# Kernel optimization log

Hardware: AMD Instinct MI355X
Metric: run time of the kernel (lower is better)

Reference implementation:

```python
import jax, jax.numpy as jnp
import numpy as np

D_K = 64
N_STEPS = 4
NEG = -1e9  # stand-in for -inf; keeps vjp NaN-free, numerically identical softmax


def setup_inputs() -> dict:
    key = jax.random.key(0)
    ks = jax.random.split(key, 12)
    B, N, D = 4, 2048, 1024
    s = 0.02
    return {
        "hidden": jax.random.normal(ks[0], (B, N, D), jnp.float32),
        "W1": jax.random.normal(ks[1], (64, D), jnp.float32) * s,
        "b1": jnp.zeros((64,), jnp.float32),
        "W2": jax.random.normal(ks[2], (28, 64), jnp.float32) * s,
        "b2": jnp.zeros((28,), jnp.float32),
        "Wq": jax.random.normal(ks[3], (D_K, 28), jnp.float32) * s,
        "Wk": jax.random.normal(ks[4], (D_K, 28), jnp.float32) * s,
        "Wc": jax.random.normal(ks[5], (1, 28), jnp.float32) * s,
        "bc": jnp.zeros((1,), jnp.float32),
        "Wv": jax.random.normal(ks[6], (D_K, D), jnp.float32) * s,
        "Wo": jax.random.normal(ks[7], (D, D_K), jnp.float32) * s,  # torch inits this to zeros; randomized for a non-trivial baseline
        "step_size": jnp.asarray(0.5, jnp.float32),
        "charge_decay": jnp.asarray(0.3, jnp.float32),
        "layer_idx": 0,
    }


def reference(hidden, W1, b1, W2, b2, Wq, Wk, Wc, bc, Wv, Wo, step_size, charge_decay, layer_idx):
    B, N, D = hidden.shape
    # features come from detached hidden in the torch code
    h_sg = jax.lax.stop_gradient(hidden)
    f = jax.nn.gelu(h_sg @ W1.T + b1, approximate=False)  # [B,N,64]
    features = jax.nn.sigmoid(f @ W2.T + b2)              # [B,N,28]
    Q = features @ Wq.T                                   # [B,N,64]
    K = features @ Wk.T                                   # [B,N,64]
    compat = jnp.einsum('bnd,bmd->bnm', Q, K) / jnp.float32(np.sqrt(D_K))
    charge = jax.nn.sigmoid(features @ Wc.T + bc)[..., 0]  # [B,N]
    causal = jnp.tril(jnp.ones((N, N), dtype=bool))
    logits = jnp.where(causal, compat, NEG)
    for _ in range(N_STEPS):
        attn = jax.nn.softmax(logits, axis=-1)            # [B,N,N]
        received = attn.sum(axis=-2)                      # [B,N]
        charge = charge * (1.0 - charge_decay * jax.nn.sigmoid(received - 1.0))
        energy = -compat * charge[:, :, None] * charge[:, None, :]
        logits = jnp.where(causal, logits - step_size * energy, NEG)
    attn = jax.nn.softmax(logits, axis=-1)
    V = hidden @ Wv.T                                     # [B,N,64]
    out = jnp.einsum('bnm,bmd->bnd', attn, V) @ Wo.T      # [B,N,D]
    return out * 0.1
```

## Files before the change

### kernel.cpp

```cpp
#include <hip/hip_runtime.h>
#include <hip/hip_bf16.h>

typedef unsigned short ushort_t;
typedef short bf16x8 __attribute__((ext_vector_type(8)));
typedef ushort_t u16x8 __attribute__((ext_vector_type(8)));
typedef float f32x4 __attribute__((ext_vector_type(4)));

#define DEV static __device__ __forceinline__

DEV float bf2f(ushort_t u) { unsigned v = ((unsigned)u) << 16; float f; __builtin_memcpy(&f, &v, 4); return f; }
DEV short f2bf(float x) { __hip_bfloat16 h = __float2bfloat16(x); short s; __builtin_memcpy(&s, &h, 2); return s; }
DEV float sigm(float x) { return 1.0f / (1.0f + __expf(-x)); }

DEV bf16x8 cvt8(float4 a0, float4 a1) {
    bf16x8 t;
    t[0] = f2bf(a0.x); t[1] = f2bf(a0.y); t[2] = f2bf(a0.z); t[3] = f2bf(a0.w);
    t[4] = f2bf(a1.x); t[5] = f2bf(a1.y); t[6] = f2bf(a1.z); t[7] = f2bf(a1.w);
    return t;
}
DEV bf16x8 ld8f(const float* __restrict__ p) {
    return cvt8(*reinterpret_cast<const float4*>(p), *reinterpret_cast<const float4*>(p + 4));
}

__global__ void k_cvt(const float* __restrict__ src, ushort_t* __restrict__ dst, int n8) {
    int i = blockIdx.x * 256 + threadIdx.x;
    if (i >= n8) return;
    const float4* p = reinterpret_cast<const float4*>(src) + (long)i * 2;
    *reinterpret_cast<bf16x8*>(dst + (long)i * 8) = cvt8(p[0], p[1]);
}

__global__ __launch_bounds__(256) void k_fv(const ushort_t* __restrict__ Hb,
        const ushort_t* __restrict__ Wcat,
        float* __restrict__ Ff, ushort_t* __restrict__ VbT) {
    int m0 = blockIdx.x * 16;
    int wave = threadIdx.x >> 6, lane = threadIdx.x & 63;
    int l16 = lane & 15, quad = lane >> 4;
    int cb = (wave & 1) * 32;
    int brow_off = (wave < 2) ? 0 : 64;
    f32x4 acc[2] = {};
    const ushort_t* arow = Hb + (long)(m0 + l16) * 1024;
    const ushort_t* brow0 = Wcat + (long)(brow_off + cb + l16) * 1024;
    const ushort_t* brow1 = Wcat + (long)(brow_off + cb + 16 + l16) * 1024;
    for (int kc = 0; kc < 1024; kc += 128) {
        bf16x8 a4[4], b04[4], b14[4];
#pragma unroll
        for (int u = 0; u < 4; u++) {
            int ko = kc + u * 32 + quad * 8;
            a4[u] = *reinterpret_cast<const bf16x8*>(arow + ko);
            b04[u] = *reinterpret_cast<const bf16x8*>(brow0 + ko);
            b14[u] = *reinterpret_cast<const bf16x8*>(brow1 + ko);
        }
#pragma unroll
        for (int u = 0; u < 4; u++) {
            acc[0] = __builtin_amdgcn_mfma_f32_16x16x32_bf16(a4[u], b04[u], acc[0], 0, 0, 0);
            acc[1] = __builtin_amdgcn_mfma_f32_16x16x32_bf16(a4[u], b14[u], acc[1], 0, 0, 0);
        }
    }
    bool isV = (wave >= 2);
#pragma unroll
    for (int c = 0; c < 2; c++)
#pragma unroll
        for (int rr = 0; rr < 4; rr++) {
            int row = m0 + quad * 4 + rr;
            int col = cb + c * 16 + l16;
            float v = acc[c][rr];
            if (!isV) Ff[row * 64 + col] = v;
            else VbT[(long)col * 8192 + row] = (ushort_t)f2bf(v);
        }
}

__global__ __launch_bounds__(256) void k_feat(const float* __restrict__ Ff,
        const float* __restrict__ b1, const float* __restrict__ W2, const float* __restrict__ b2,
        const float* __restrict__ Wq, const float* __restrict__ Wk,
        const float* __restrict__ Wc, const float* __restrict__ bc,
        ushort_t* __restrict__ Qb, ushort_t* __restrict__ Kb,
        float* __restrict__ charge0, float* __restrict__ received) {
    __shared__ float w2L[28 * 65], wqL[64 * 29], wkL[64 * 29], wcL[28], b2L[28];
    __shared__ float fL[4][64], featL[4][28];
    int tid = threadIdx.x;
    for (int i = tid; i < 28 * 64; i += 256) w2L[(i >> 6) * 65 + (i & 63)] = W2[i];
    for (int i = tid; i < 64 * 28; i += 256) {
        int r = i / 28, c = i - r * 28;
        wqL[r * 29 + c] = Wq[i];
        wkL[r * 29 + c] = Wk[i];
    }
    if (tid < 28) { wcL[tid] = Wc[tid]; b2L[tid] = b2[tid]; }
    __syncthreads();
    int w = tid >> 6, lane = tid & 63;
    float b1v = b1[lane];
    float bcv = bc[0];
    for (int it = 0; it < 8; it++) {
        int row = blockIdx.x * 32 + it * 4 + w;
        float x = Ff[row * 64 + lane] + b1v;
        fL[w][lane] = 0.5f * x * (1.0f + erff(x * 0.70710678118654752f));
        __syncthreads();
        if (lane < 28) {
            float s = b2L[lane];
#pragma unroll
            for (int j = 0; j < 64; j++) s += fL[w][j] * w2L[lane * 65 + j];
            featL[w][lane] = sigm(s);
        }
        __syncthreads();
        float q = 0.f, k = 0.f;
#pragma unroll
        for (int i = 0; i < 28; i++) {
            float fv = featL[w][i];
            q += fv * wqL[lane * 29 + i];
            k += fv * wkL[lane * 29 + i];
        }
        Qb[row * 64 + lane] = (ushort_t)f2bf(q * 0.125f);
        Kb[row * 64 + lane] = (ushort_t)f2bf(k);
        if (lane == 0) {
            float c = bcv;
#pragma unroll
            for (int i = 0; i < 28; i++) c += featL[w][i] * wcL[i];
            charge0[row] = sigm(c);
            received[row] = 0.f;
        }
        __syncthreads();
    }
}

DEV void tri_decode(int r, int& ti, int& tj) {
    int t = (int)((sqrtf(8.f * (float)r + 1.f) - 1.f) * 0.5f);
    while ((t + 1) * (t + 2) / 2 <= r) t++;
    while (t * (t + 1) / 2 > r) t--;
    ti = t;
    tj = r - t * (t + 1) / 2;
}

__global__ __launch_bounds__(256) void k_compat(const ushort_t* __restrict__ Qb,
                                                const ushort_t* __restrict__ Kb,
                                                ushort_t* __restrict__ compat) {
    int bid = blockIdx.x;
    int b = bid / 136, r = bid % 136, ti, tj;
    tri_decode(r, ti, tj);
    int wave = threadIdx.x >> 6, lane = threadIdx.x & 63;
    int l16 = lane & 15, quad = lane >> 4;
    int rbase = b * 2048 + ti * 128 + wave * 32;
    int cbase = b * 2048 + tj * 128;
    f32x4 acc[2][8] = {};
#pragma unroll
    for (int kc = 0; kc < 64; kc += 32) {
        int ko = kc + quad * 8;
        bf16x8 af[2], bf[8];
#pragma unroll
        for (int f = 0; f < 2; f++) af[f] = *reinterpret_cast<const bf16x8*>(Qb + (long)(rbase + f * 16 + l16) * 64 + ko);
#pragma unroll
        for (int f = 0; f < 8; f++) bf[f] = *reinterpret_cast<const bf16x8*>(Kb + (long)(cbase + f * 16 + l16) * 64 + ko);
#pragma unroll
        for (int i = 0; i < 2; i++)
#pragma unroll
            for (int j = 0; j < 8; j++)
                acc[i][j] = __builtin_amdgcn_mfma_f32_16x16x32_bf16(af[i], bf[j], acc[i][j], 0, 0, 0);
    }
    int colt = tj * 128;
#pragma unroll
    for (int i = 0; i < 2; i++)
#pragma unroll
        for (int j = 0; j < 8; j++)
#pragma unroll
            for (int rr = 0; rr < 4; rr++) {
                long rowg = rbase + i * 16 + quad * 4 + rr;
                int col = colt + j * 16 + l16;
                compat[rowg * 2048 + col] = (ushort_t)f2bf(acc[i][j][rr]);
            }
}

template <int T>
__global__ __launch_bounds__(256) void k_rowstats(const ushort_t* __restrict__ compat,
        const float4* __restrict__ charges4, const float* __restrict__ stepp,
        float* __restrict__ Lp) {
    int bid = blockIdx.x;
    int z = bid & 1;
    int b = (bid >> 1) & 3;
    int rt = 127 - (bid >> 3);
    int w = threadIdx.x >> 6, lane = threadIdx.x & 63;
    int rw0 = rt * 16 + w * 4;
    int colbase = b * 2048;
    if (z == 1 && rt < 64) {
        if (lane == 0) {
#pragma unroll
            for (int r = 0; r < 4; r++) Lp[8192 + colbase + rw0 + r] = 0.f;
        }
        return;
    }
    float step = stepp[0];
    float rfx[4] = {}, rfy[4] = {}, rfz[4] = {}, rfw[4] = {};
    if (T > 0) {
#pragma unroll
        for (int r = 0; r < 4; r++) {
            float4 c4 = charges4[colbase + rw0 + r];
            rfx[r] = step * c4.x;
            if (T > 1) rfy[r] = step * c4.y;
            if (T > 2) rfz[r] = step * c4.z;
            if (T > 3) rfw[r] = step * c4.w;
        }
    }
    const ushort_t* crow0 = compat + (long)(colbase + rw0) * 2048;
    int nmax = rw0 + 3;
    float S[4] = {0.f, 0.f, 0.f, 0.f};
#pragma unroll
    for (int it = 0; it < 2; it++) {
        int mb = z * 1024 + it * 512 + lane * 8;
        if (mb > nmax) continue;
        u16x8 cv[4];
#pragma unroll
        for (int r = 0; r < 4; r++) cv[r] = *reinterpret_cast<const u16x8*>(crow0 + (long)r * 2048 + mb);
        float4 ch[8];
        if (T > 0) {
#pragma unroll
            for (int j = 0; j < 8; j++) ch[j] = charges4[colbase + mb + j];
        }
#pragma unroll
        for (int j = 0; j < 8; j++) {
#pragma unroll
            for (int r = 0; r < 4; r++) {
                float sg = 1.f;
                if (T > 0) sg += rfx[r] * ch[j].x;
                if (T > 1) sg += rfy[r] * ch[j].y;
                if (T > 2) sg += rfz[r] * ch[j].z;
                if (T > 3) sg += rfw[r] * ch[j].w;
                float e = (mb + j <= rw0 + r) ? __expf(bf2f(cv[r][j]) * sg) : 0.f;
                S[r] += e;
            }
        }
    }
#pragma unroll
    for (int off = 32; off > 0; off >>= 1) {
#pragma unroll
        for (int r = 0; r < 4; r++) S[r] += __shfl_down(S[r], off);
    }
    if (lane == 0) {
#pragma unroll
        for (int r = 0; r < 4; r++) Lp[z * 8192 + colbase + rw0 + r] = S[r];
    }
}

template <int T>
__global__ __launch_bounds__(256) void k_colsum(const ushort_t* __restrict__ compat,
        const float4* __restrict__ charges4, const float* __restrict__ stepp,
        const float* __restrict__ Lp, float* __restrict__ received) {
    __shared__ float nvx[32], nvy[32], nvz[32], nvw[32], nLi[32];
    __shared__ float sums[16][136];
    int bid = blockIdx.x;
    int b = bid / 544, rem = bid % 544;
    int q = rem & 3, r = rem >> 2, ti, tj;
    tri_decode(r, ti, tj);
    int tid = threadIdx.x;
    float step = stepp[0];
    if (tid < 32) {
        int nid = b * 2048 + ti * 128 + q * 32 + tid;
        nLi[tid] = 1.0f / fmaxf(Lp[nid] + Lp[8192 + nid], 1e-30f);
        if (T > 0) {
            float4 cn = charges4[nid];
            nvx[tid] = step * cn.x;
            if (T > 1) nvy[tid] = step * cn.y;
            if (T > 2) nvz[tid] = step * cn.z;
            if (T > 3) nvw[tid] = step * cn.w;
        }
    }
    __syncthreads();
    int cg = tid & 15, ng = tid >> 4;
    int m0 = tj * 128 + cg * 8;
    long mid0 = (long)b * 2048 + m0;
    float4 cm[8];
    if (T > 0) {
#pragma unroll
        for (int j = 0; j < 8; j++) cm[j] = charges4[mid0 + j];
    }
    bool diag = (ti == tj);
    u16x8 cva[2];
    int nla[2];
#pragma unroll
    for (int t2 = 0; t2 < 2; t2++) {
        nla[t2] = q * 32 + ng + t2 * 16;
        long nid = (long)b * 2048 + ti * 128 + nla[t2];
        cva[t2] = *reinterpret_cast<const u16x8*>(compat + nid * 2048 + m0);
    }
    float acc[8] = {};
#pragma unroll
    for (int t2 = 0; t2 < 2; t2++) {
        int nloc = ng + t2 * 16;
        float Li = nLi[nloc];
        float ax = (T > 0) ? nvx[nloc] : 0.f;
        float ay = (T > 1) ? nvy[nloc] : 0.f;
        float az = (T > 2) ? nvz[nloc] : 0.f;
        float aw = (T > 3) ? nvw[nloc] : 0.f;
        int nglob = ti * 128 + nla[t2];
#pragma unroll
        for (int j = 0; j < 8; j++) {
            float sg = 1.f;
            if (T > 0) sg += ax * cm[j].x;
            if (T > 1) sg += ay * cm[j].y;
            if (T > 2) sg += az * cm[j].z;
            if (T > 3) sg += aw * cm[j].w;
            float p = __expf(bf2f(cva[t2][j]) * sg) * Li;
            if (!diag || m0 + j <= nglob) acc[j] += p;
        }
    }
#pragma unroll
    for (int j = 0; j < 8; j++) sums[ng][cg * 8 + j] = acc[j];
    __syncthreads();
    if (tid < 128) {
        float s = 0.f;
#pragma unroll
        for (int g = 0; g < 16; g++) s += sums[g][tid];
        atomicAdd(&received[b * 2048 + tj * 128 + tid], s);
    }
}

template <int T>
__global__ void k_charge(float* __restrict__ received, const float* __restrict__ charge0,
                         float4* __restrict__ charges4, const float* __restrict__ decayp) {
    int i = blockIdx.x * 256 + threadIdx.x;
    if (i >= 8192) return;
    float decay = decayp[0];
    float rcv = received[i];
    float sg = 1.0f / (1.0f + __expf(1.0f - rcv));
    float prev = (T == 1) ? charge0[i] : ((const float*)&charges4[i])[T - 2];
    ((float*)&charges4[i])[T - 1] = prev * (1.f - decay * sg);
    received[i] = 0.f;
}

__global__ __launch_bounds__(256) void k_pv(const ushort_t* __restrict__ compat,
        const float4* __restrict__ charges4, const float* __restrict__ stepp,
        const ushort_t* __restrict__ VbT, float* __restrict__ Oacc) {
    __shared__ float accL[3][64][17];
    __shared__ float ssL[4][16];
    int bid = blockIdx.x;
    int b = bid & 3, rtile = 127 - (bid >> 2);
    int r0 = rtile * 16;
    int w = threadIdx.x >> 6, lane = threadIdx.x & 63;
    int l16 = lane & 15, quad = lane >> 4;
    int rowl = r0 + l16;
    int rid = b * 2048 + rowl;
    float step = stepp[0];
    float4 c4 = charges4[rid];
    float rx = step * c4.x, ry = step * c4.y, rz = step * c4.z, rw = step * c4.w;
    const ushort_t* crow = compat + (long)rid * 2048;
    f32x4 acc[4] = {};
    float Ss = 0.f;
    int colend = r0 + 16;
    for (int kc = w * 32; kc < colend; kc += 128) {
        int mk = kc + quad * 8;
        u16x8 cv = *reinterpret_cast<const u16x8*>(crow + mk);
        const float4* chp = charges4 + b * 2048 + mk;
        bf16x8 pf;
#pragma unroll
        for (int j = 0; j < 8; j++) {
            float4 ch = chp[j];
            float sg = 1.f + rx * ch.x + ry * ch.y + rz * ch.z + rw * ch.w;
            float p = (mk + j <= rowl) ? __expf(bf2f(cv[j]) * sg) : 0.f;
            Ss += p;
            pf[j] = f2bf(p);
        }
        bf16x8 vf[4];
#pragma unroll
        for (int f = 0; f < 4; f++)
            vf[f] = *reinterpret_cast<const bf16x8*>(VbT + (long)(f * 16 + l16) * 8192 + b * 2048 + mk);
#pragma unroll
        for (int f = 0; f < 4; f++)
            acc[f] = __builtin_amdgcn_mfma_f32_16x16x32_bf16(pf, vf[f], acc[f], 0, 0, 0);
    }
    Ss += __shfl_xor(Ss, 16);
    Ss += __shfl_xor(Ss, 32);
    if (quad == 0) ssL[w][l16] = Ss;
    if (w > 0) {
#pragma unroll
        for (int f = 0; f < 4; f++)
#pragma unroll
            for (int rr = 0; rr < 4; rr++)
                accL[w - 1][lane][f * 4 + rr] = acc[f][rr];
    }
    __syncthreads();
    if (w == 0) {
#pragma unroll
        for (int f = 0; f < 4; f++)
#pragma unroll
            for (int rr = 0; rr < 4; rr++)
                acc[f][rr] += accL[0][lane][f * 4 + rr] + accL[1][lane][f * 4 + rr] + accL[2][lane][f * 4 + rr];
        float Sinv[4];
#pragma unroll
        for (int rr = 0; rr < 4; rr++) {
            int idx = quad * 4 + rr;
            float st = ssL[0][idx] + ssL[1][idx] + ssL[2][idx] + ssL[3][idx];
            Sinv[rr] = 1.f / fmaxf(st, 1e-30f);
        }
#pragma unroll
        for (int f = 0; f < 4; f++)
#pragma unroll
            for (int rr = 0; rr < 4; rr++) {
                int row = r0 + quad * 4 + rr;
                Oacc[(long)(b * 2048 + row) * 64 + f * 16 + l16] = acc[f][rr] * Sinv[rr];
            }
    }
}

__global__ __launch_bounds__(256) void k_oproj(const float* __restrict__ Oacc,
                                               const float* __restrict__ Wo,
                                               float* __restrict__ out) {
    int mt = blockIdx.x & 63, nt = blockIdx.x >> 6;
    int wave = threadIdx.x >> 6, lane = threadIdx.x & 63;
    int wm = wave >> 1, wn = wave & 1;
    int l16 = lane & 15, quad = lane >> 4;
    int row0 = mt * 128 + wm * 64;
    int col0 = nt * 128 + wn * 64;
    f32x4 acc[4][4] = {};
#pragma unroll
    for (int kc = 0; kc < 64; kc += 32) {
        int ko = kc + quad * 8;
        bf16x8 af[4], bfm[4];
#pragma unroll
        for (int f = 0; f < 4; f++) af[f] = ld8f(Oacc + (long)(row0 + f * 16 + l16) * 64 + ko);
#pragma unroll
        for (int f = 0; f < 4; f++) bfm[f] = ld8f(Wo + (long)(col0 + f * 16 + l16) * 64 + ko);
#pragma unroll
        for (int i = 0; i < 4; i++)
#pragma unroll
            for (int j = 0; j < 4; j++)
                acc[i][j] = __builtin_amdgcn_mfma_f32_16x16x32_bf16(af[i], bfm[j], acc[i][j], 0, 0, 0);
    }
#pragma unroll
    for (int i = 0; i < 4; i++)
#pragma unroll
        for (int j = 0; j < 4; j++)
#pragma unroll
            for (int rr = 0; rr < 4; rr++) {
                long rowg = row0 + i * 16 + quad * 4 + rr;
                int colg = col0 + j * 16 + l16;
                out[rowg * 1024 + colg] = acc[i][j][rr] * 0.1f;
            }
}

extern "C" void kernel_launch(void* const* d_in, const int* in_sizes, int n_in,
                              void* d_out, int out_size, void* d_ws, size_t ws_size,
                              hipStream_t stream) {
    const float* hidden = (const float*)d_in[0];
    const float* W1 = (const float*)d_in[1];
    const float* b1 = (const float*)d_in[2];
    const float* W2 = (const float*)d_in[3];
    const float* b2 = (const float*)d_in[4];
    const float* Wq = (const float*)d_in[5];
    const float* Wk = (const float*)d_in[6];
    const float* Wc = (const float*)d_in[7];
    const float* bc = (const float*)d_in[8];
    const float* Wv = (const float*)d_in[9];
    const float* Wo = (const float*)d_in[10];
    const float* stepp = (const float*)d_in[11];
    const float* decayp = (const float*)d_in[12];

    char* ws = (char*)d_ws;
    size_t off = 0;
    auto alloc = [&](size_t bytes) {
        void* p = ws + off;
        off += (bytes + 255) & ~(size_t)255;
        return p;
    };
    ushort_t* compat = (ushort_t*)alloc(8192UL * 2048 * 2);
    ushort_t* Hb = (ushort_t*)alloc(8192UL * 1024 * 2);
    ushort_t* Wcat = (ushort_t*)alloc(128UL * 1024 * 2);
    float* Ff = (float*)alloc(8192UL * 64 * 4);
    ushort_t* Qb = (ushort_t*)alloc(8192UL * 64 * 2);
    ushort_t* Kb = (ushort_t*)alloc(8192UL * 64 * 2);
    ushort_t* VbT = (ushort_t*)alloc(64UL * 8192 * 2);
    float* Oacc = (float*)alloc(8192UL * 64 * 4);
    float4* charges4 = (float4*)alloc(8192UL * 16);
    float* charge0 = (float*)alloc(8192UL * 4);
    float* Lp = (float*)alloc(2UL * 8192 * 4);
    float* received = (float*)alloc(8192UL * 4);
    (void)ws_size; (void)in_sizes; (void)n_in; (void)out_size;

    k_cvt<<<4096, 256, 0, stream>>>(hidden, Hb, 8192 * 1024 / 8);
    k_cvt<<<32, 256, 0, stream>>>(W1, Wcat, 64 * 1024 / 8);
    k_cvt<<<32, 256, 0, stream>>>(Wv, Wcat + 64 * 1024, 64 * 1024 / 8);
    k_fv<<<512, 256, 0, stream>>>(Hb, Wcat, Ff, VbT);
    k_feat<<<256, 256, 0, stream>>>(Ff, b1, W2, b2, Wq, Wk, Wc, bc, Qb, Kb, charge0, received);
    k_compat<<<544, 256, 0, stream>>>(Qb, Kb, compat);

    k_rowstats<0><<<1024, 256, 0, stream>>>(compat, charges4, stepp, Lp);
    k_colsum<0><<<2176, 256, 0, stream>>>(compat, charges4, stepp, Lp, received);
    k_charge<1><<<32, 256, 0, stream>>>(received, charge0, charges4, decayp);

    k_rowstats<1><<<1024, 256, 0, stream>>>(compat, charges4, stepp, Lp);
    k_colsum<1><<<2176, 256, 0, stream>>>(compat, charges4, stepp, Lp, received);
    k_charge<2><<<32, 256, 0, stream>>>(received, charge0, charges4, decayp);

    k_rowstats<2><<<1024, 256, 0, stream>>>(compat, charges4, stepp, Lp);
    k_colsum<2><<<2176, 256, 0, stream>>>(compat, charges4, stepp, Lp, received);
    k_charge<3><<<32, 256, 0, stream>>>(received, charge0, charges4, decayp);

    k_rowstats<3><<<1024, 256, 0, stream>>>(compat, charges4, stepp, Lp);
    k_colsum<3><<<2176, 256, 0, stream>>>(compat, charges4, stepp, Lp, received);
    k_charge<4><<<32, 256, 0, stream>>>(received, charge0, charges4, decayp);

    k_pv<<<512, 256, 0, stream>>>(compat, charges4, stepp, VbT, Oacc);
    k_oproj<<<512, 256, 0, stream>>>(Oacc, Wo, (float*)d_out);
}
```

Measured before the change: 291.9 us.

## Coarsen rowstats and colsum blocks and merge conversion launches

Three conversion launches are merged into a single k_cvt kernel. k_rowstats now handles 16 rows per block, with the four waves splitting the columns. It reduces through shared memory and writes one clamped row sum, which removes the two-partial Lp buffer. k_colsum now handles a full 128x128 tile per block, looping over 8 row groups, so there are four times fewer blocks and atomics and the per-column charges are reused across rows. The cost is fewer blocks, which means less parallelism and latency hiding, plus a serial loop inside each block.

```diff
diff --git a/kernel.cpp b/kernel.cpp
--- a/kernel.cpp
+++ b/kernel.cpp
@@ -22,11 +22,17 @@
     return cvt8(*reinterpret_cast<const float4*>(p), *reinterpret_cast<const float4*>(p + 4));
 }
 
-__global__ void k_cvt(const float* __restrict__ src, ushort_t* __restrict__ dst, int n8) {
-    int i = blockIdx.x * 256 + threadIdx.x;
-    if (i >= n8) return;
-    const float4* p = reinterpret_cast<const float4*>(src) + (long)i * 2;
-    *reinterpret_cast<bf16x8*>(dst + (long)i * 8) = cvt8(p[0], p[1]);
+__global__ void k_cvt(const float* __restrict__ h, const float* __restrict__ W1,
+                      const float* __restrict__ Wv, ushort_t* __restrict__ Hb,
+                      ushort_t* __restrict__ Wcat) {
+    long i = (long)blockIdx.x * 256 + threadIdx.x;
+    const float* src;
+    ushort_t* dst;
+    if (i < 1048576) { src = h + i * 8; dst = Hb + i * 8; }
+    else if (i < 1056768) { long j = i - 1048576; src = W1 + j * 8; dst = Wcat + j * 8; }
+    else { long j = i - 1056768; src = Wv + j * 8; dst = Wcat + 65536 + j * 8; }
+    const float4* p = reinterpret_cast<const float4*>(src);
+    *reinterpret_cast<bf16x8*>(dst) = cvt8(p[0], p[1]);
 }
 
 __global__ __launch_bounds__(256) void k_fv(const ushort_t* __restrict__ Hb,
@@ -170,88 +176,95 @@
 template <int T>
 __global__ __launch_bounds__(256) void k_rowstats(const ushort_t* __restrict__ compat,
         const float4* __restrict__ charges4, const float* __restrict__ stepp,
-        float* __restrict__ Lp) {
+        float* __restrict__ Lrow) {
+    __shared__ float lsum[4][16];
     int bid = blockIdx.x;
-    int z = bid & 1;
-    int b = (bid >> 1) & 3;
-    int rt = 127 - (bid >> 3);
+    int b = bid & 3, rt = 127 - (bid >> 2);
     int w = threadIdx.x >> 6, lane = threadIdx.x & 63;
-    int rw0 = rt * 16 + w * 4;
+    int r0 = rt * 16;
     int colbase = b * 2048;
-    if (z == 1 && rt < 64) {
-        if (lane == 0) {
-#pragma unroll
-            for (int r = 0; r < 4; r++) Lp[8192 + colbase + rw0 + r] = 0.f;
-        }
-        return;
-    }
+    int mb = w * 512 + lane * 8;
     float step = stepp[0];
-    float rfx[4] = {}, rfy[4] = {}, rfz[4] = {}, rfw[4] = {};
-    if (T > 0) {
-#pragma unroll
-        for (int r = 0; r < 4; r++) {
-            float4 c4 = charges4[colbase + rw0 + r];
-            rfx[r] = step * c4.x;
-            if (T > 1) rfy[r] = step * c4.y;
-            if (T > 2) rfz[r] = step * c4.z;
-            if (T > 3) rfw[r] = step * c4.w;
-        }
-    }
-    const ushort_t* crow0 = compat + (long)(colbase + rw0) * 2048;
-    int nmax = rw0 + 3;
-    float S[4] = {0.f, 0.f, 0.f, 0.f};
-#pragma unroll
-    for (int it = 0; it < 2; it++) {
-        int mb = z * 1024 + it * 512 + lane * 8;
-        if (mb > nmax) continue;
-        u16x8 cv[4];
-#pragma unroll
-        for (int r = 0; r < 4; r++) cv[r] = *reinterpret_cast<const u16x8*>(crow0 + (long)r * 2048 + mb);
-        float4 ch[8];
+    float S[16];
+#pragma unroll
+    for (int i = 0; i < 16; i++) S[i] = 0.f;
+    if (mb <= r0 + 15) {
+        float chx[8] = {}, chy[8] = {}, chz[8] = {}, chw[8] = {};
         if (T > 0) {
 #pragma unroll
-            for (int j = 0; j < 8; j++) ch[j] = charges4[colbase + mb + j];
-        }
-#pragma unroll
-        for (int j = 0; j < 8; j++) {
-#pragma unroll
-            for (int r = 0; r < 4; r++) {
-                float sg = 1.f;
-                if (T > 0) sg += rfx[r] * ch[j].x;
-                if (T > 1) sg += rfy[r] * ch[j].y;
-                if (T > 2) sg += rfz[r] * ch[j].z;
-                if (T > 3) sg += rfw[r] * ch[j].w;
-                float e = (mb + j <= rw0 + r) ? __expf(bf2f(cv[r][j]) * sg) : 0.f;
-                S[r] += e;
+            for (int j = 0; j < 8; j++) {
+                float4 c = charges4[colbase + mb + j];
+                chx[j] = c.x;
+                if (T > 1) chy[j] = c.y;
+                if (T > 2) chz[j] = c.z;
+                if (T > 3) chw[j] = c.w;
             }
         }
+        const ushort_t* cbase = compat + (long)(colbase + r0) * 2048 + mb;
+        for (int rb = 0; rb < 4; rb++) {
+            int rr0 = r0 + rb * 4;
+            if (mb > rr0 + 3) continue;
+            u16x8 cv[4];
+#pragma unroll
+            for (int rr = 0; rr < 4; rr++)
+                cv[rr] = *reinterpret_cast<const u16x8*>(cbase + (long)(rb * 4 + rr) * 2048);
+            float rfx[4] = {}, rfy[4] = {}, rfz[4] = {}, rfw[4] = {};
+            if (T > 0) {
+#pragma unroll
+                for (int rr = 0; rr < 4; rr++) {
+                    float4 c4 = charges4[colbase + rr0 + rr];
+                    rfx[rr] = step * c4.x;
+                    if (T > 1) rfy[rr] = step * c4.y;
+                    if (T > 2) rfz[rr] = step * c4.z;
+                    if (T > 3) rfw[rr] = step * c4.w;
+                }
+            }
+#pragma unroll
+            for (int rr = 0; rr < 4; rr++) {
+                int n = rr0 + rr;
+#pragma unroll
+                for (int j = 0; j < 8; j++) {
+                    float sg = 1.f;
+                    if (T > 0) sg += rfx[rr] * chx[j];
+                    if (T > 1) sg += rfy[rr] * chy[j];
+                    if (T > 2) sg += rfz[rr] * chz[j];
+                    if (T > 3) sg += rfw[rr] * chw[j];
+                    float e = (mb + j <= n) ? __expf(bf2f(cv[rr][j]) * sg) : 0.f;
+                    S[rb * 4 + rr] += e;
+                }
+            }
+        }
     }
 #pragma unroll
     for (int off = 32; off > 0; off >>= 1) {
 #pragma unroll
-        for (int r = 0; r < 4; r++) S[r] += __shfl_down(S[r], off);
+        for (int i = 0; i < 16; i++) S[i] += __shfl_down(S[i], off);
     }
     if (lane == 0) {
 #pragma unroll
-        for (int r = 0; r < 4; r++) Lp[z * 8192 + colbase + rw0 + r] = S[r];
+        for (int i = 0; i < 16; i++) lsum[w][i] = S[i];
+    }
+    __syncthreads();
+    if (threadIdx.x < 16) {
+        float s = lsum[0][threadIdx.x] + lsum[1][threadIdx.x] + lsum[2][threadIdx.x] + lsum[3][threadIdx.x];
+        Lrow[colbase + r0 + threadIdx.x] = fmaxf(s, 1e-30f);
     }
 }
 
 template <int T>
 __global__ __launch_bounds__(256) void k_colsum(const ushort_t* __restrict__ compat,
         const float4* __restrict__ charges4, const float* __restrict__ stepp,
-        const float* __restrict__ Lp, float* __restrict__ received) {
-    __shared__ float nvx[32], nvy[32], nvz[32], nvw[32], nLi[32];
+        const float* __restrict__ Lrow, float* __restrict__ received) {
+    __shared__ float nLi[128], nvx[128], nvy[128], nvz[128], nvw[128];
     __shared__ float sums[16][136];
     int bid = blockIdx.x;
-    int b = bid / 544, rem = bid % 544;
-    int q = rem & 3, r = rem >> 2, ti, tj;
+    int b = bid & 3, r = bid >> 2, ti, tj;
     tri_decode(r, ti, tj);
     int tid = threadIdx.x;
     float step = stepp[0];
-    if (tid < 32) {
-        int nid = b * 2048 + ti * 128 + q * 32 + tid;
-        nLi[tid] = 1.0f / fmaxf(Lp[nid] + Lp[8192 + nid], 1e-30f);
+    if (tid < 128) {
+        int nid = b * 2048 + ti * 128 + tid;
+        nLi[tid] = 1.0f / Lrow[nid];
         if (T > 0) {
             float4 cn = charges4[nid];
             nvx[tid] = step * cn.x;
@@ -263,39 +276,37 @@
     __syncthreads();
     int cg = tid & 15, ng = tid >> 4;
     int m0 = tj * 128 + cg * 8;
-    long mid0 = (long)b * 2048 + m0;
-    float4 cm[8];
+    float cmx[8] = {}, cmy[8] = {}, cmz[8] = {}, cmw[8] = {};
     if (T > 0) {
 #pragma unroll
-        for (int j = 0; j < 8; j++) cm[j] = charges4[mid0 + j];
+        for (int j = 0; j < 8; j++) {
+            float4 c = charges4[b * 2048 + m0 + j];
+            cmx[j] = c.x;
+            if (T > 1) cmy[j] = c.y;
+            if (T > 2) cmz[j] = c.z;
+            if (T > 3) cmw[j] = c.w;
+        }
     }
     bool diag = (ti == tj);
-    u16x8 cva[2];
-    int nla[2];
-#pragma unroll
-    for (int t2 = 0; t2 < 2; t2++) {
-        nla[t2] = q * 32 + ng + t2 * 16;
-        long nid = (long)b * 2048 + ti * 128 + nla[t2];
-        cva[t2] = *reinterpret_cast<const u16x8*>(compat + nid * 2048 + m0);
-    }
+    const ushort_t* cbase = compat + (long)(b * 2048 + ti * 128) * 2048 + m0;
     float acc[8] = {};
-#pragma unroll
-    for (int t2 = 0; t2 < 2; t2++) {
-        int nloc = ng + t2 * 16;
+    for (int nb = 0; nb < 8; nb++) {
+        int nloc = nb * 16 + ng;
+        u16x8 cv = *reinterpret_cast<const u16x8*>(cbase + (long)nloc * 2048);
         float Li = nLi[nloc];
         float ax = (T > 0) ? nvx[nloc] : 0.f;
         float ay = (T > 1) ? nvy[nloc] : 0.f;
         float az = (T > 2) ? nvz[nloc] : 0.f;
         float aw = (T > 3) ? nvw[nloc] : 0.f;
-        int nglob = ti * 128 + nla[t2];
+        int nglob = ti * 128 + nloc;
 #pragma unroll
         for (int j = 0; j < 8; j++) {
             float sg = 1.f;
-            if (T > 0) sg += ax * cm[j].x;
-            if (T > 1) sg += ay * cm[j].y;
-            if (T > 2) sg += az * cm[j].z;
-            if (T > 3) sg += aw * cm[j].w;
-            float p = __expf(bf2f(cva[t2][j]) * sg) * Li;
+            if (T > 0) sg += ax * cmx[j];
+            if (T > 1) sg += ay * cmy[j];
+            if (T > 2) sg += az * cmz[j];
+            if (T > 3) sg += aw * cmw[j];
+            float p = __expf(bf2f(cv[j]) * sg) * Li;
             if (!diag || m0 + j <= nglob) acc[j] += p;
         }
     }
@@ -467,31 +478,29 @@
     float* Oacc = (float*)alloc(8192UL * 64 * 4);
     float4* charges4 = (float4*)alloc(8192UL * 16);
     float* charge0 = (float*)alloc(8192UL * 4);
-    float* Lp = (float*)alloc(2UL * 8192 * 4);
+    float* Lrow = (float*)alloc(8192UL * 4);
     float* received = (float*)alloc(8192UL * 4);
     (void)ws_size; (void)in_sizes; (void)n_in; (void)out_size;
 
-    k_cvt<<<4096, 256, 0, stream>>>(hidden, Hb, 8192 * 1024 / 8);
-    k_cvt<<<32, 256, 0, stream>>>(W1, Wcat, 64 * 1024 / 8);
-    k_cvt<<<32, 256, 0, stream>>>(Wv, Wcat + 64 * 1024, 64 * 1024 / 8);
+    k_cvt<<<4160, 256, 0, stream>>>(hidden, W1, Wv, Hb, Wcat);
     k_fv<<<512, 256, 0, stream>>>(Hb, Wcat, Ff, VbT);
     k_feat<<<256, 256, 0, stream>>>(Ff, b1, W2, b2, Wq, Wk, Wc, bc, Qb, Kb, charge0, received);
     k_compat<<<544, 256, 0, stream>>>(Qb, Kb, compat);
 
-    k_rowstats<0><<<1024, 256, 0, stream>>>(compat, charges4, stepp, Lp);
-    k_colsum<0><<<2176, 256, 0, stream>>>(compat, charges4, stepp, Lp, received);
+    k_rowstats<0><<<512, 256, 0, stream>>>(compat, charges4, stepp, Lrow);
+    k_colsum<0><<<544, 256, 0, stream>>>(compat, charges4, stepp, Lrow, received);
     k_charge<1><<<32, 256, 0, stream>>>(received, charge0, charges4, decayp);
 
-    k_rowstats<1><<<1024, 256, 0, stream>>>(compat, charges4, stepp, Lp);
-    k_colsum<1><<<2176, 256, 0, stream>>>(compat, charges4, stepp, Lp, received);
+    k_rowstats<1><<<512, 256, 0, stream>>>(compat, charges4, stepp, Lrow);
+    k_colsum<1><<<544, 256, 0, stream>>>(compat, charges4, stepp, Lrow, received);
     k_charge<2><<<32, 256, 0, stream>>>(received, charge0, charges4, decayp);
 
-    k_rowstats<2><<<1024, 256, 0, stream>>>(compat, charges4, stepp, Lp);
-    k_colsum<2><<<2176, 256, 0, stream>>>(compat, charges4, stepp, Lp, received);
+    k_rowstats<2><<<512, 256, 0, stream>>>(compat, charges4, stepp, Lrow);
+    k_colsum<2><<<544, 256, 0, stream>>>(compat, charges4, stepp, Lrow, received);
     k_charge<3><<<32, 256, 0, stream>>>(received, charge0, charges4, decayp);
 
-    k_rowstats<3><<<1024, 256, 0, stream>>>(compat, charges4, stepp, Lp);
-    k_colsum<3><<<2176, 256, 0, stream>>>(compat, charges4, stepp, Lp, received);
+    k_rowstats<3><<<512, 256, 0, stream>>>(compat, charges4, stepp, Lrow);
+    k_colsum<3><<<544, 256, 0, stream>>>(compat, charges4, stepp, Lrow, received);
     k_charge<4><<<32, 256, 0, stream>>>(received, charge0, charges4, decayp);
 
     k_pv<<<512, 256, 0, stream>>>(compat, charges4, stepp, VbT, Oacc);
```

After: 277.5 us. 5.0% less time.
